# Optimization experiments

Hardware: AMD Instinct MI355X
Metric: run time of the kernel (lower is better)

## Reference

```python
import jax, jax.numpy as jnp
import numpy as np

B, S, D = 16, 2048, 512
E, TOP_K = 8, 2
H = 4 * D  # expert hidden dim


def setup_inputs() -> dict:
    key = jax.random.key(0)
    ks = jax.random.split(key, 8)
    x = jax.random.normal(ks[0], (B, S, D), dtype=jnp.float32)
    gate_w = jax.random.normal(ks[1], (D, E), dtype=jnp.float32) * 0.02
    gate_b = jnp.zeros((E,), dtype=jnp.float32)
    w1 = jax.random.normal(ks[2], (E, D, H), dtype=jnp.float32) * 0.02
    b1 = jnp.zeros((E, H), dtype=jnp.float32)
    w2 = jax.random.normal(ks[3], (E, H, D), dtype=jnp.float32) * 0.02
    b2 = jnp.zeros((E, D), dtype=jnp.float32)
    return {"x": x, "gate_w": gate_w, "gate_b": gate_b,
            "w1": w1, "b1": b1, "w2": w2, "b2": b2}


def reference(x, gate_w, gate_b, w1, b1, w2, b2):
    # Sample-level top-k routing (mean pooling over sequence).
    b, s, d = x.shape
    e = gate_b.shape[0]
    pooled = x.mean(axis=1)                       # [B, D]
    logits = pooled @ gate_w + gate_b             # [B, E]
    top_v, top_i = jax.lax.top_k(logits, TOP_K)   # [B, K]
    weights = jax.nn.softmax(top_v, axis=-1)      # [B, K]
    # Dense per-sample-per-expert combine weight; zero for unselected experts,
    # which makes the dense expert evaluation below mathematically identical
    # to the masked gather/scatter in the torch module.
    w_full = jnp.zeros((b, e), dtype=x.dtype).at[jnp.arange(b)[:, None], top_i].add(weights)
    out = jnp.zeros_like(x)
    for ex in range(e):  # small fixed expert loop
        h = jax.nn.gelu(x @ w1[ex] + b1[ex], approximate=False)  # torch GELU default = exact erf
        y = h @ w2[ex] + b2[ex]  # Dropout(0.1) is identity in eval mode
        out = out + y * w_full[:, ex][:, None, None]
    return out
```

## Files before the change

kernel.cpp:

```cpp
#include <hip/hip_runtime.h>
#include <hip/hip_bf16.h>
#include <math.h>

#define B_ 16
#define S_ 2048
#define D_ 512
#define E_ 8
#define H_ 2048

typedef __bf16 bf16_t;
typedef __bf16 bf16x8 __attribute__((ext_vector_type(8)));
typedef __bf16 bf16x4v __attribute__((ext_vector_type(4)));
typedef float f32x4 __attribute__((ext_vector_type(4)));

__device__ __forceinline__ void gload_lds16(const void* g, void* l) {
  __builtin_amdgcn_global_load_lds((const __attribute__((address_space(1))) void*)g,
                                   (__attribute__((address_space(3))) void*)l,
                                   16, 0, 0);
}

#define BAR() __builtin_amdgcn_s_barrier()
#define LGKM0() do { asm volatile("s_waitcnt lgkmcnt(0)" ::: "memory"); \
                     __builtin_amdgcn_sched_barrier(0); } while (0)
#define LGKMW() asm volatile("s_waitcnt lgkmcnt(0)" ::: "memory")
#define VM4() asm volatile("s_waitcnt vmcnt(4)" ::: "memory")
#define VM0() asm volatile("s_waitcnt vmcnt(0)" ::: "memory")
#define PRIO1() __builtin_amdgcn_s_setprio(1)
#define PRIO0() __builtin_amdgcn_s_setprio(0)

__device__ __forceinline__ float fast_gelu(float v) {
  const float t = 1.5957691216f * v * (1.0f + 0.044715f * v * v);
  return v * __builtin_amdgcn_rcpf(1.0f + __expf(-t));
}

__global__ void prep_kernel(const float* __restrict__ x, bf16_t* __restrict__ xbf,
                            float* __restrict__ pool,
                            const float* __restrict__ w1, bf16_t* __restrict__ w1t,
                            const float* __restrict__ w2, bf16_t* __restrict__ w2t) {
  const int id = blockIdx.x;
  const int tid = threadIdx.x;
  if (id < 256) {
    const int ch = id & 15, b = id >> 4;
    const int cg = tid & 127;
    const int rg = tid >> 7;
    const size_t base = ((size_t)b * S_ + (size_t)ch * 128 + rg * 32) * D_ + cg * 4;
    const float* xp = x + base;
    bf16_t* op = xbf + base;
    float s0 = 0.f, s1 = 0.f, s2 = 0.f, s3 = 0.f;
#pragma unroll 4
    for (int r = 0; r < 32; ++r) {
      float4 v = *reinterpret_cast<const float4*>(xp + (size_t)r * D_);
      s0 += v.x; s1 += v.y; s2 += v.z; s3 += v.w;
      bf16x4v o;
      o[0] = (bf16_t)v.x; o[1] = (bf16_t)v.y; o[2] = (bf16_t)v.z; o[3] = (bf16_t)v.w;
      *reinterpret_cast<bf16x4v*>(op + (size_t)r * D_) = o;
    }
    float* pp = pool + ((size_t)b * 64 + ch * 4 + rg) * D_ + cg * 4;
    pp[0] = s0; pp[1] = s1; pp[2] = s2; pp[3] = s3;
    return;
  }
  __shared__ bf16_t tile[128][72];
  int t = id - 256;
  const float* in; bf16_t* outp; int R, C, r0, c0;
  if (t < 1024) {
    const int e = t >> 7, u = t & 127;
    R = D_; C = H_;
    r0 = (u >> 4) * 64; c0 = (u & 15) * 128;
    in = w1 + (size_t)e * R * C; outp = w1t + (size_t)e * R * C;
  } else {
    t -= 1024;
    const int e = t >> 7, u = t & 127;
    R = H_; C = D_;
    r0 = (u >> 2) * 64; c0 = (u & 3) * 128;
    in = w2 + (size_t)e * R * C; outp = w2t + (size_t)e * R * C;
  }
  const int tx = tid & 15, ty = (tid >> 4) & 15, hf = tid >> 8;
#pragma unroll
  for (int i = 0; i < 4; ++i) {
    const int r = r0 + ty + i * 16;
    float4 v = *reinterpret_cast<const float4*>(&in[(size_t)r * C + c0 + hf * 64 + tx * 4]);
    tile[hf * 64 + tx * 4 + 0][ty + i * 16] = (bf16_t)v.x;
    tile[hf * 64 + tx * 4 + 1][ty + i * 16] = (bf16_t)v.y;
    tile[hf * 64 + tx * 4 + 2][ty + i * 16] = (bf16_t)v.z;
    tile[hf * 64 + tx * 4 + 3][ty + i * 16] = (bf16_t)v.w;
  }
  __syncthreads();
#pragma unroll
  for (int i = 0; i < 4; ++i) {
    const int c = c0 + hf * 64 + ty + i * 16;
    bf16x4v o;
    o[0] = tile[hf * 64 + ty + i * 16][tx * 4 + 0];
    o[1] = tile[hf * 64 + ty + i * 16][tx * 4 + 1];
    o[2] = tile[hf * 64 + ty + i * 16][tx * 4 + 2];
    o[3] = tile[hf * 64 + ty + i * 16][tx * 4 + 3];
    *reinterpret_cast<bf16x4v*>(&outp[(size_t)c * R + r0 + tx * 4]) = o;
  }
}

__global__ void gate_kernel(const float* __restrict__ pool, const float* __restrict__ gw,
                            const float* __restrict__ gb, int* __restrict__ route_e,
                            float* __restrict__ route_w) {
  const int b = blockIdx.x;
  const int d = threadIdx.x;
  float p = 0.f;
#pragma unroll
  for (int c = 0; c < 64; ++c) p += pool[((size_t)b * 64 + c) * D_ + d];
  p *= (1.0f / (float)S_);

  __shared__ float red[512];
  __shared__ float logits[E_];
  for (int e = 0; e < E_; ++e) {
    red[d] = p * gw[d * E_ + e];
    __syncthreads();
    for (int off = 256; off > 0; off >>= 1) {
      if (d < off) red[d] += red[d + off];
      __syncthreads();
    }
    if (d == 0) logits[e] = red[0] + gb[e];
    __syncthreads();
  }
  if (d == 0) {
    int i0 = 0; float v0 = logits[0];
    for (int e = 1; e < E_; ++e) if (logits[e] > v0) { v0 = logits[e]; i0 = e; }
    int i1 = -1; float v1 = -3.0e38f;
    for (int e = 0; e < E_; ++e) if (e != i0 && logits[e] > v1) { v1 = logits[e]; i1 = e; }
    const float z = expf(v1 - v0);
    const float inv = 1.0f / (1.0f + z);
    route_e[2 * b] = i0; route_e[2 * b + 1] = i1;
    route_w[2 * b] = inv; route_w[2 * b + 1] = z * inv;
  }
}

#define GEMM_THREAD_CONSTS() \
  const int tid = threadIdx.x; \
  const int lane = tid & 63; \
  const int wave = tid >> 6; \
  const int wr = wave >> 2; \
  const int wc = wave & 3; \
  const int fl = lane & 15; \
  const int hi = (lane >> 4) & 3; \
  const int flb = fl * 128; \
  const int xorv = (fl & 7) << 4; \
  const int koff0 = (hi * 16) ^ xorv; \
  const int koff1 = (64 + hi * 16) ^ xorv; \
  const int r0s = tid >> 3; \
  const int g0s = ((tid & 7) ^ (r0s & 7)) << 3; \
  const int r1s = 64 + (tid >> 3); \
  const int g1s = ((tid & 7) ^ (r1s & 7)) << 3;

#define STAGE_HALF(g, ld, row0, col0, lo) do { \
  gload_lds16((g) + (size_t)((row0) + r0s) * (ld) + (col0) + g0s, smem + (lo) + tid * 16); \
  gload_lds16((g) + (size_t)((row0) + r1s) * (ld) + (col0) + g1s, smem + (lo) + 8192 + tid * 16); \
} while (0)

#define RD_A(mh) do { \
  const char* _pA = smem + ((((t) & 1) * 2 + wr) << 14); \
  _Pragma("unroll") for (int mq = 0; mq < 4; ++mq) { \
    a[mq][0] = *reinterpret_cast<const bf16x8*>(_pA + (mh) * 8192 + mq * 2048 + flb + koff0); \
    a[mq][1] = *reinterpret_cast<const bf16x8*>(_pA + (mh) * 8192 + mq * 2048 + flb + koff1); \
  } } while (0)

#define RD_B(nh) do { \
  const char* _pB = smem + 65536 + ((((t) & 1) * 2 + (wc >> 1)) << 14) + ((wc & 1) << 13); \
  _Pragma("unroll") for (int nq = 0; nq < 2; ++nq) { \
    bb[nh][nq][0] = *reinterpret_cast<const bf16x8*>(_pB + (nh) * 4096 + nq * 2048 + flb + koff0); \
    bb[nh][nq][1] = *reinterpret_cast<const bf16x8*>(_pB + (nh) * 4096 + nq * 2048 + flb + koff1); \
  } } while (0)

#define MFMA_Q(mh, nh) do { \
  _Pragma("unroll") for (int mq = 0; mq < 4; ++mq) \
  _Pragma("unroll") for (int nq = 0; nq < 2; ++nq) { \
    acc[(mh)*4+mq][(nh)*2+nq] = __builtin_amdgcn_mfma_f32_16x16x32_bf16( \
        a[mq][0], bb[nh][nq][0], acc[(mh)*4+mq][(nh)*2+nq], 0, 0, 0); \
    acc[(mh)*4+mq][(nh)*2+nq] = __builtin_amdgcn_mfma_f32_16x16x32_bf16( \
        a[mq][1], bb[nh][nq][1], acc[(mh)*4+mq][(nh)*2+nq], 0, 0, 0); \
  } } while (0)

__global__ __launch_bounds__(512, 2) void gemm1_kernel(
    const bf16_t* __restrict__ xbf, const bf16_t* __restrict__ w1t,
    const float* __restrict__ b1, const int* __restrict__ route_e,
    bf16_t* __restrict__ h_ws, int g0) {
  __shared__ alignas(16) char smem[131072];
  const int nwg = gridDim.x;
  const int id = blockIdx.x;
  const int swz = (id & 7) * (nwg >> 3) + (id >> 3);
  const int lg = swz >> 6;
  const int tile = swz & 63;
  const int m0 = (tile >> 3) * 256;
  const int n0 = (tile & 7) * 256;
  const int g = g0 + lg;
  const int b = g >> 1;
  const int e = route_e[g];
  const bf16_t* Ax = xbf + (size_t)b * S_ * D_;
  const bf16_t* Bw = w1t + (size_t)e * H_ * D_;
  bf16_t* C = h_ws + (size_t)lg * S_ * H_;

  GEMM_THREAD_CONSTS();

  f32x4 acc[8][4];
#pragma unroll
  for (int i = 0; i < 8; ++i)
#pragma unroll
    for (int j = 0; j < 4; ++j) acc[i][j] = f32x4{0.f, 0.f, 0.f, 0.f};
  bf16x8 a[4][2], bb[2][2][2];

#define ST_A1(tt, hh) STAGE_HALF(Ax, D_, m0 + (hh) * 128, (tt) * 64, ((((tt) & 1) * 2 + (hh)) << 14))
#define ST_B1(tt, hh) STAGE_HALF(Bw, D_, n0 + (hh) * 128, (tt) * 64, 65536 + ((((tt) & 1) * 2 + (hh)) << 14))

  const int NT = D_ / 64;
  ST_A1(0, 0); ST_A1(0, 1); ST_B1(0, 0); ST_B1(0, 1);
  ST_B1(1, 0); ST_B1(1, 1);
  VM4(); BAR();

  for (int t = 0; t < NT; ++t) {
    RD_A(0); RD_B(0);
    if (t + 1 < NT) ST_A1(t + 1, 0);
    BAR(); LGKM0(); PRIO1(); MFMA_Q(0, 0); PRIO0(); BAR();
    RD_B(1);
    if (t + 1 < NT) ST_A1(t + 1, 1);
    BAR(); LGKM0(); PRIO1(); MFMA_Q(0, 1); PRIO0(); BAR();
    RD_A(1);
    if (t + 2 < NT) ST_B1(t + 2, 0);
    BAR(); LGKM0(); PRIO1(); MFMA_Q(1, 0); PRIO0(); BAR();
    if (t + 2 < NT) ST_B1(t + 2, 1);
    if (t < NT - 2) { VM4(); } else if (t == NT - 2) { VM0(); }
    BAR(); PRIO1(); MFMA_Q(1, 1); PRIO0(); BAR();
  }
#undef ST_A1
#undef ST_B1

  const int rb2 = hi * 4;
#pragma unroll
  for (int ni = 0; ni < 4; ++ni) {
    const int col = wc * 64 + ni * 16 + fl;
    const float bias = b1[e * H_ + n0 + col];
    const int cb = col * 2;
#pragma unroll
    for (int mi = 0; mi < 8; ++mi) {
#pragma unroll
      for (int j = 0; j < 4; ++j) {
        const int row = wr * 128 + mi * 16 + rb2 + j;
        const float v = acc[mi][ni][j] + bias;
        const int ad = (row << 9) + (cb ^ (((row >> 2) & 3) << 5));
        *reinterpret_cast<bf16_t*>(smem + ad) = (bf16_t)fast_gelu(v);
      }
    }
  }
  LGKMW(); BAR();
#pragma unroll
  for (int i = 0; i < 16; ++i) {
    const int byte = i * 8192 + tid * 16;
    const int row = byte >> 9;
    const int colb = byte & 511;
    const int ad = (row << 9) + (colb ^ (((row >> 2) & 3) << 5));
    const bf16x8 vv = *reinterpret_cast<const bf16x8*>(smem + ad);
    *reinterpret_cast<bf16x8*>((char*)C + ((size_t)(m0 + row) * H_ + n0) * 2 + colb) = vv;
  }
}

__global__ __launch_bounds__(512, 2) void gemm2_kernel(
    const bf16_t* __restrict__ h_ws, const bf16_t* __restrict__ w2t,
    const float* __restrict__ b2, const int* __restrict__ route_e,
    const float* __restrict__ route_w, float* __restrict__ out, int b0) {
  __shared__ alignas(16) char smem[131072];
  const int nwg = gridDim.x;
  const int id = blockIdx.x;
  const int swz = (id & 7) * (nwg >> 3) + (id >> 3);
  const int lb = swz >> 4;
  const int tile = swz & 15;
  const int m0 = (tile >> 1) * 256;
  const int n0 = (tile & 1) * 256;
  const int smp = b0 + lb;
  const int e0 = route_e[2 * smp], e1 = route_e[2 * smp + 1];
  const float wg0 = route_w[2 * smp], wg1 = route_w[2 * smp + 1];
  const float ratio = wg1 / wg0;
  const bf16_t* Ae1 = h_ws + (size_t)(lb * 2 + 1) * S_ * H_;
  const bf16_t* Ae0 = h_ws + (size_t)(lb * 2 + 0) * S_ * H_;
  const bf16_t* Be1 = w2t + (size_t)e1 * D_ * H_;
  const bf16_t* Be0 = w2t + (size_t)e0 * D_ * H_;

  GEMM_THREAD_CONSTS();

  f32x4 acc[8][4];
#pragma unroll
  for (int i = 0; i < 8; ++i)
#pragma unroll
    for (int j = 0; j < 4; ++j) acc[i][j] = f32x4{0.f, 0.f, 0.f, 0.f};
  bf16x8 a[4][2], bb[2][2][2];

#define ST_A2(tt, hh) do { const bf16_t* _ab = ((tt) < 32) ? Ae1 : Ae0; \
  STAGE_HALF(_ab, H_, m0 + (hh) * 128, ((tt) & 31) * 64, ((((tt) & 1) * 2 + (hh)) << 14)); } while (0)
#define ST_B2(tt, hh) do { const bf16_t* _bbp = ((tt) < 32) ? Be1 : Be0; \
  STAGE_HALF(_bbp, H_, n0 + (hh) * 128, ((tt) & 31) * 64, 65536 + ((((tt) & 1) * 2 + (hh)) << 14)); } while (0)

  const int NT = 64;
  ST_A2(0, 0); ST_A2(0, 1); ST_B2(0, 0); ST_B2(0, 1);
  ST_B2(1, 0); ST_B2(1, 1);
  VM4(); BAR();

  for (int t = 0; t < NT; ++t) {
    RD_A(0); RD_B(0);
    if (t + 1 < NT) ST_A2(t + 1, 0);
    BAR(); LGKM0(); PRIO1(); MFMA_Q(0, 0); PRIO0(); BAR();
    RD_B(1);
    if (t + 1 < NT) ST_A2(t + 1, 1);
    BAR(); LGKM0(); PRIO1(); MFMA_Q(0, 1); PRIO0(); BAR();
    RD_A(1);
    if (t + 2 < NT) ST_B2(t + 2, 0);
    BAR(); LGKM0(); PRIO1(); MFMA_Q(1, 0); PRIO0(); BAR();
    if (t + 2 < NT) ST_B2(t + 2, 1);
    if (t < NT - 2) { VM4(); } else if (t == NT - 2) { VM0(); }
    BAR(); PRIO1(); MFMA_Q(1, 1); PRIO0();
    if (t == 31) {
#pragma unroll
      for (int i = 0; i < 8; ++i)
#pragma unroll
        for (int j = 0; j < 4; ++j) acc[i][j] = acc[i][j] * ratio;
    }
    BAR();
  }
#undef ST_A2
#undef ST_B2

  const int rb2 = hi * 4;
  float* Co = out + (size_t)smp * S_ * D_;
#pragma unroll
  for (int p = 0; p < 2; ++p) {
#pragma unroll
    for (int ni = 0; ni < 4; ++ni) {
      const int col = wc * 64 + ni * 16 + fl;
      const float wb = wg0 * b2[e0 * D_ + n0 + col] + wg1 * b2[e1 * D_ + n0 + col];
      const int cb = col * 4;
#pragma unroll
      for (int mq = 0; mq < 4; ++mq) {
        const int mi = 4 * p + mq;
#pragma unroll
        for (int j = 0; j < 4; ++j) {
          const int row = wr * 128 + mi * 16 + rb2 + j;
          const int lrow = (row & 63) + ((row >> 7) << 6);
          const int ad = (lrow << 10) + (cb ^ (((row >> 2) & 1) << 6));
          *reinterpret_cast<float*>(smem + ad) = wg0 * acc[mi][ni][j] + wb;
        }
      }
    }
    LGKMW(); BAR();
#pragma unroll
    for (int i = 0; i < 16; ++i) {
      const int byte = i * 8192 + tid * 16;
      const int lrow = byte >> 10;
      const int colb = byte & 1023;
      const int row = (lrow & 63) + ((lrow >> 6) << 7) + p * 64;
      const int ad = (lrow << 10) + (colb ^ (((row >> 2) & 1) << 6));
      const f32x4 vv = *reinterpret_cast<const f32x4*>(smem + ad);
      *reinterpret_cast<f32x4*>((char*)Co + ((size_t)(m0 + row) * D_ + n0) * 4 + colb) = vv;
    }
    LGKMW(); BAR();
  }
}

extern "C" void kernel_launch(void* const* d_in, const int* in_sizes, int n_in,
                              void* d_out, int out_size, void* d_ws, size_t ws_size,
                              hipStream_t stream) {
  const float* x      = (const float*)d_in[0];
  const float* gate_w = (const float*)d_in[1];
  const float* gate_b = (const float*)d_in[2];
  const float* w1     = (const float*)d_in[3];
  const float* b1     = (const float*)d_in[4];
  const float* w2     = (const float*)d_in[5];
  const float* b2     = (const float*)d_in[6];
  float* out = (float*)d_out;
  char* ws = (char*)d_ws;

  bf16_t* xbf    = (bf16_t*)(ws);
  bf16_t* w1t    = (bf16_t*)(ws + 33554432);
  bf16_t* w2t    = (bf16_t*)(ws + 50331648);
  float*  pool   = (float*)(ws + 67108864);
  int*    route_e = (int*)(ws + 69206016);
  float*  route_w = (float*)(ws + 69206144);
  const size_t h_off = 69206272;
  bf16_t* h_ws   = (bf16_t*)(ws + h_off);

  const size_t per_b = (size_t)2 * S_ * H_ * sizeof(bf16_t);
  size_t avail = (ws_size > h_off) ? (ws_size - h_off) : 0;
  int nb = (int)(avail / per_b);
  if (nb < 1) nb = 1;
  if (nb > B_) nb = B_;

  prep_kernel<<<2304, 512, 0, stream>>>(x, xbf, pool, w1, w1t, w2, w2t);
  gate_kernel<<<B_, 512, 0, stream>>>(pool, gate_w, gate_b, route_e, route_w);

  for (int b0 = 0; b0 < B_; b0 += nb) {
    const int cb = (B_ - b0 < nb) ? (B_ - b0) : nb;
    gemm1_kernel<<<64 * cb * 2, 512, 0, stream>>>(xbf, w1t, b1, route_e, h_ws, b0 * 2);
    gemm2_kernel<<<16 * cb, 512, 0, stream>>>(h_ws, w2t, b2, route_e, route_w, out, b0);
  }
}
```

Baseline: 469.3 us.

## Make gemm1 blocks sweep all hidden-dim tiles with an in-loop GELU epilogue

Each gemm1 workgroup now owns a 256-row strip of one (sample, expert) pair and loops over all eight 256-wide hidden-dim tiles in a single 64-step K/N pipeline, instead of launching one workgroup per 256x256 output tile. After every eighth step it applies bias and GELU, writes the tile to global memory through LDS scratch in four chunks, and zeroes the accumulators. The grid shrinks eightfold, which cuts per-block prologue and epilogue overhead and keeps the software pipeline running across tiles. In exchange there are fewer workgroups to fill the GPU, and the epilogue's barriers now stall the MFMA pipeline inside the main loop.

```diff
diff --git a/kernel.cpp b/kernel.cpp
--- a/kernel.cpp
+++ b/kernel.cpp
@@ -184,10 +184,9 @@
   const int nwg = gridDim.x;
   const int id = blockIdx.x;
   const int swz = (id & 7) * (nwg >> 3) + (id >> 3);
-  const int lg = swz >> 6;
-  const int tile = swz & 63;
-  const int m0 = (tile >> 3) * 256;
-  const int n0 = (tile & 7) * 256;
+  const int lg = swz >> 3;
+  const int ms = swz & 7;
+  const int m0 = ms * 256;
   const int g = g0 + lg;
   const int b = g >> 1;
   const int e = route_e[g];
@@ -204,14 +203,17 @@
     for (int j = 0; j < 4; ++j) acc[i][j] = f32x4{0.f, 0.f, 0.f, 0.f};
   bf16x8 a[4][2], bb[2][2][2];
 
-#define ST_A1(tt, hh) STAGE_HALF(Ax, D_, m0 + (hh) * 128, (tt) * 64, ((((tt) & 1) * 2 + (hh)) << 14))
-#define ST_B1(tt, hh) STAGE_HALF(Bw, D_, n0 + (hh) * 128, (tt) * 64, 65536 + ((((tt) & 1) * 2 + (hh)) << 14))
-
-  const int NT = D_ / 64;
+#define ST_A1(tt, hh) STAGE_HALF(Ax, D_, m0 + (hh) * 128, ((tt) & 7) * 64, \
+                                 ((((tt) & 1) * 2 + (hh)) << 14))
+#define ST_B1(tt, hh) STAGE_HALF(Bw, D_, ((tt) >> 3) * 256 + (hh) * 128, ((tt) & 7) * 64, \
+                                 65536 + ((((tt) & 1) * 2 + (hh)) << 14))
+
+  const int NT = 64;
   ST_A1(0, 0); ST_A1(0, 1); ST_B1(0, 0); ST_B1(0, 1);
   ST_B1(1, 0); ST_B1(1, 1);
   VM4(); BAR();
 
+  const int rb2 = hi * 4;
   for (int t = 0; t < NT; ++t) {
     RD_A(0); RD_B(0);
     if (t + 1 < NT) ST_A1(t + 1, 0);
@@ -225,37 +227,55 @@
     if (t + 2 < NT) ST_B1(t + 2, 1);
     if (t < NT - 2) { VM4(); } else if (t == NT - 2) { VM0(); }
     BAR(); PRIO1(); MFMA_Q(1, 1); PRIO0(); BAR();
+
+    if ((t & 7) == 7) {
+      const int nt = t >> 3;
+      const int n0e = nt * 256;
+      char* scr = smem + 32768;
+      float biasr[4];
+#pragma unroll
+      for (int ni = 0; ni < 4; ++ni)
+        biasr[ni] = b1[e * H_ + n0e + wc * 64 + ni * 16 + fl];
+#pragma unroll
+      for (int p = 0; p < 4; ++p) {
+#pragma unroll
+        for (int ni = 0; ni < 4; ++ni) {
+          const int cb = (wc * 64 + ni * 16 + fl) * 2;
+#pragma unroll
+          for (int u = 0; u < 2; ++u) {
+            const int mi = 2 * p + u;
+#pragma unroll
+            for (int j = 0; j < 4; ++j) {
+              const int lr = wr * 32 + u * 16 + rb2 + j;
+              const float v = acc[mi][ni][j] + biasr[ni];
+              const int ad = (lr << 9) + (cb ^ (((lr >> 2) & 3) << 5));
+              *reinterpret_cast<bf16_t*>(scr + ad) = (bf16_t)fast_gelu(v);
+            }
+          }
+        }
+        LGKMW(); BAR();
+#pragma unroll
+        for (int i = 0; i < 4; ++i) {
+          const int byte = i * 8192 + tid * 16;
+          const int lr = byte >> 9;
+          const int colb = byte & 511;
+          const int ad = (lr << 9) + (colb ^ (((lr >> 2) & 3) << 5));
+          const bf16x8 vv = *reinterpret_cast<const bf16x8*>(scr + ad);
+          const int grow = (lr >> 5) * 128 + (2 * p + ((lr >> 4) & 1)) * 16 + (lr & 15);
+          *reinterpret_cast<bf16x8*>((char*)C + ((size_t)(m0 + grow) * H_ + n0e) * 2 + colb) = vv;
+        }
+        LGKMW(); BAR();
+      }
+      if (t + 1 < NT) {
+#pragma unroll
+        for (int i = 0; i < 8; ++i)
+#pragma unroll
+          for (int j = 0; j < 4; ++j) acc[i][j] = f32x4{0.f, 0.f, 0.f, 0.f};
+      }
+    }
   }
 #undef ST_A1
 #undef ST_B1
-
-  const int rb2 = hi * 4;
-#pragma unroll
-  for (int ni = 0; ni < 4; ++ni) {
-    const int col = wc * 64 + ni * 16 + fl;
-    const float bias = b1[e * H_ + n0 + col];
-    const int cb = col * 2;
-#pragma unroll
-    for (int mi = 0; mi < 8; ++mi) {
-#pragma unroll
-      for (int j = 0; j < 4; ++j) {
-        const int row = wr * 128 + mi * 16 + rb2 + j;
-        const float v = acc[mi][ni][j] + bias;
-        const int ad = (row << 9) + (cb ^ (((row >> 2) & 3) << 5));
-        *reinterpret_cast<bf16_t*>(smem + ad) = (bf16_t)fast_gelu(v);
-      }
-    }
-  }
-  LGKMW(); BAR();
-#pragma unroll
-  for (int i = 0; i < 16; ++i) {
-    const int byte = i * 8192 + tid * 16;
-    const int row = byte >> 9;
-    const int colb = byte & 511;
-    const int ad = (row << 9) + (colb ^ (((row >> 2) & 3) << 5));
-    const bf16x8 vv = *reinterpret_cast<const bf16x8*>(smem + ad);
-    *reinterpret_cast<bf16x8*>((char*)C + ((size_t)(m0 + row) * H_ + n0) * 2 + colb) = vv;
-  }
 }
 
 __global__ __launch_bounds__(512, 2) void gemm2_kernel(
@@ -391,7 +411,7 @@
 
   for (int b0 = 0; b0 < B_; b0 += nb) {
     const int cb = (B_ - b0 < nb) ? (B_ - b0) : nb;
-    gemm1_kernel<<<64 * cb * 2, 512, 0, stream>>>(xbf, w1t, b1, route_e, h_ws, b0 * 2);
+    gemm1_kernel<<<8 * cb * 2, 512, 0, stream>>>(xbf, w1t, b1, route_e, h_ws, b0 * 2);
     gemm2_kernel<<<16 * cb, 512, 0, stream>>>(h_ws, w2t, b2, route_e, route_w, out, b0);
   }
 }
```

Result: slower. 605.0 us (+28.9%).
